# Kernel tuning notes

Measured on AMD Instinct MI355X. Metric: run time of the kernel, lower is better.

The kernel has to match this reference:

```python
import jax, jax.numpy as jnp
import numpy as np

# Model dims (match init_kwargs)
HID = 1024   # hidden_size
H   = 16     # num_heads
DK  = 64     # head_dim (key)
DV  = 128    # head value dim = int(head_dim * expand_v)
VAL = H * DV # value_dim = 2048
CONV = 4     # short conv kernel size
EPS = 1e-6
NORM_EPS = 1e-5


def _causal_conv_silu(x, w):
    # x: [B,T,C], w: [C,K] depthwise causal conv, no bias, silu activation
    T = x.shape[1]
    K = w.shape[1]
    xp = jnp.pad(x, ((0, 0), (K - 1, 0), (0, 0)))
    y = sum(xp[:, i:i + T, :] * w[:, i] for i in range(K))
    return jax.nn.silu(y)


def setup_inputs() -> dict:
    key = jax.random.key(0)
    ks = jax.random.split(key, 16)
    s = 0.02
    rn = lambda k, sh: jax.random.normal(k, sh, jnp.float32)
    return {
        'hidden_states': rn(ks[0], (1, 2048, HID)),
        'norm_w': jnp.ones((HID,), jnp.float32),
        'q_w': rn(ks[1], (H * DK, HID)) * s,
        'k_w': rn(ks[2], (H * DK, HID)) * s,
        'v_w': rn(ks[3], (VAL, HID)) * s,
        'a_w': rn(ks[4], (H, HID)) * s,
        'b_w': rn(ks[5], (H, HID)) * s,
        'g_w': rn(ks[6], (VAL, HID)) * s,
        'dt_bias': jax.random.uniform(ks[7], (H,), jnp.float32, -2.0, 0.0),
        'A_log': jnp.log(jax.random.uniform(ks[8], (H,), jnp.float32, 1.0, 8.0)),
        'conv_q_w': rn(ks[9], (H * DK, CONV)) * 0.2,
        'conv_k_w': rn(ks[10], (H * DK, CONV)) * 0.2,
        'conv_v_w': rn(ks[11], (VAL, CONV)) * 0.2,
        'o_norm_w': jnp.ones((DV,), jnp.float32),
        'o_proj_w': rn(ks[12], (HID, VAL)) * s,
        'out_proj_w': rn(ks[13], (HID, HID)) * s,
    }


def reference(hidden_states, norm_w, q_w, k_w, v_w, a_w, b_w, g_w, dt_bias,
              A_log, conv_q_w, conv_k_w, conv_v_w, o_norm_w, o_proj_w, out_proj_w):
    B, T, D = hidden_states.shape
    # RMSNorm
    x = hidden_states * jax.lax.rsqrt(
        jnp.mean(hidden_states * hidden_states, -1, keepdims=True) + EPS) * norm_w

    # projections + causal depthwise short conv + silu
    q = _causal_conv_silu(x @ q_w.T, conv_q_w).reshape(B, T, H, DK)
    k = _causal_conv_silu(x @ k_w.T, conv_k_w).reshape(B, T, H, DK)
    v = _causal_conv_silu(x @ v_w.T, conv_v_w).reshape(B, T, H, DV)

    beta = jax.nn.sigmoid(x @ b_w.T)                       # [B,T,H]
    g = -jnp.exp(A_log) * jax.nn.softplus(x @ a_w.T + dt_bias)  # [B,T,H] log-decay

    # rank-1 DC removal on keys: (I - 1 1^T / DK) k, i.e. subtract per-head mean
    k = k - jnp.mean(k, -1, keepdims=True)

    # L2 normalize q, k along head dim; scale q
    q = q * jax.lax.rsqrt(jnp.sum(q * q, -1, keepdims=True) + EPS)
    k = k * jax.lax.rsqrt(jnp.sum(k * k, -1, keepdims=True) + EPS)
    q = q * (DK ** -0.5)

    # gated delta-rule recurrence over time (time-major scan)
    qT = q.transpose(1, 0, 2, 3)
    kT = k.transpose(1, 0, 2, 3)
    vT = v.transpose(1, 0, 2, 3)
    bT = beta.transpose(1, 0, 2)
    gT = g.transpose(1, 0, 2)

    def step(S, inp):
        qt, kt, vt, bt, gt = inp              # S: [B,H,DK,DV]
        S = S * jnp.exp(gt)[..., None, None]
        v_new = (vt - jnp.einsum('bhk,bhkv->bhv', kt, S)) * bt[..., None]
        S = S + jnp.einsum('bhk,bhv->bhkv', kt, v_new)
        o = jnp.einsum('bhk,bhkv->bhv', qt, S)
        return S, o

    S0 = jnp.zeros((B, H, DK, DV), x.dtype)
    _, oT = jax.lax.scan(step, S0, (qT, kT, vT, bT, gT))
    o = oT.transpose(1, 0, 2, 3)                           # [B,T,H,DV]

    # gated RMSNorm on output heads
    gate = (x @ g_w.T).reshape(B, T, H, DV)
    o = o * jax.lax.rsqrt(jnp.mean(o * o, -1, keepdims=True) + NORM_EPS) * o_norm_w
    o = o * jax.nn.silu(gate)

    o = o.reshape(B, T, VAL) @ o_proj_w.T                  # [B,T,HID]
    return o @ out_proj_w.T
```

## Files before the change

kernel.cpp:

```cpp
#include <hip/hip_runtime.h>
#include <math.h>

#define TT 2048
#define S72 72

typedef __bf16 bf16;
typedef __bf16 bf16x8 __attribute__((ext_vector_type(8)));
typedef __bf16 bf16x4v __attribute__((ext_vector_type(4)));
typedef __bf16 bf16x2v __attribute__((ext_vector_type(2)));
typedef float f32x4 __attribute__((ext_vector_type(4)));

__device__ __forceinline__ float wredsum(float v) {
#pragma unroll
  for (int off = 32; off > 0; off >>= 1) v += __shfl_xor(v, off, 64);
  return v;
}
__device__ __forceinline__ float sigmoidf_(float x) { return 1.f / (1.f + __expf(-x)); }

__global__ __launch_bounds__(256) void k_rmsnorm(const float* __restrict__ h,
    const float* __restrict__ nw, const float* __restrict__ aw,
    const float* __restrict__ bw, const float* __restrict__ dtb,
    const float* __restrict__ alog, bf16* __restrict__ xb,
    float* __restrict__ graw, float* __restrict__ btb) {
  int t = blockIdx.x, tid = threadIdx.x;
  float4 hv = *(const float4*)(h + (size_t)t*1024 + tid*4);
  float ss = hv.x*hv.x + hv.y*hv.y + hv.z*hv.z + hv.w*hv.w;
  __shared__ float red[4];
  __shared__ __align__(16) float xs[1024];
  float wsum = wredsum(ss);
  if ((tid & 63) == 0) red[tid >> 6] = wsum;
  __syncthreads();
  float tot = red[0] + red[1] + red[2] + red[3];
  float rs = rsqrtf(tot * (1.f/1024.f) + 1e-6f);
  float4 w4 = *(const float4*)(nw + tid*4);
  float4 y;
  y.x = hv.x*rs*w4.x; y.y = hv.y*rs*w4.y; y.z = hv.z*rs*w4.z; y.w = hv.w*rs*w4.w;
  *(float4*)(xs + tid*4) = y;
  bf16x4v b; b[0]=(bf16)y.x; b[1]=(bf16)y.y; b[2]=(bf16)y.z; b[3]=(bf16)y.w;
  *(bf16x4v*)(xb + (size_t)t*1024 + tid*4) = b;
  __syncthreads();
  int wave = tid >> 6, lane = tid & 63;
  const float4* x4 = (const float4*)xs;
#pragma unroll
  for (int hi = 0; hi < 4; ++hi) {
    int hh = wave*4 + hi;
    float sa = 0.f, sb = 0.f;
#pragma unroll
    for (int i = 0; i < 4; ++i) {
      float4 xv = x4[i*64 + lane];
      float4 av = *(const float4*)(aw + hh*1024 + i*256 + lane*4);
      float4 bv = *(const float4*)(bw + hh*1024 + i*256 + lane*4);
      sa += xv.x*av.x + xv.y*av.y + xv.z*av.z + xv.w*av.w;
      sb += xv.x*bv.x + xv.y*bv.y + xv.z*bv.z + xv.w*bv.w;
    }
    sa = wredsum(sa); sb = wredsum(sb);
    if (lane == 0) {
      float ap = sa + dtb[hh];
      float sp = (ap > 20.f) ? ap : log1pf(expf(ap));
      graw[t*16 + hh] = -expf(alog[hh]) * sp;
      btb[t*16 + hh] = 1.f / (1.f + expf(-sb));
    }
  }
}

__global__ void k_castw(const float* __restrict__ qw, const float* __restrict__ kw,
    const float* __restrict__ vw, const float* __restrict__ gw,
    const float* __restrict__ opw, const float* __restrict__ ow,
    bf16* qwb, bf16* kwb, bf16* vwb, bf16* gwb, bf16* opwb, bf16* owb) {
  for (long u = (long)blockIdx.x*256 + threadIdx.x; u < 2359296; u += (long)gridDim.x*256) {
    const float* src; bf16* dst; long l;
    if      (u <  262144) { src=qw;  dst=qwb;  l=u; }
    else if (u <  524288) { src=kw;  dst=kwb;  l=u-262144; }
    else if (u < 1048576) { src=vw;  dst=vwb;  l=u-524288; }
    else if (u < 1572864) { src=gw;  dst=gwb;  l=u-1048576; }
    else if (u < 2097152) { src=opw; dst=opwb; l=u-1572864; }
    else                  { src=ow;  dst=owb;  l=u-2097152; }
    float4 s = *(const float4*)(src + l*4);
    bf16x4v b; b[0]=(bf16)s.x; b[1]=(bf16)s.y; b[2]=(bf16)s.z; b[3]=(bf16)s.w;
    *(bf16x4v*)(dst + l*4) = b;
  }
}

template <typename OutT>
__device__ __forceinline__ void gemm_body(const bf16* __restrict__ A,
    const bf16* __restrict__ B, OutT* __restrict__ C, int N, int K, int m0, int n0) {
  __shared__ bf16 As[2][128*32];
  __shared__ bf16 Bs[2][128*32];
  const int tid = threadIdx.x, lane = tid & 63, wave = tid >> 6;
  const int wm = (wave >> 1) * 64, wn = (wave & 1) * 64;
  const int srow = wave*16 + (lane >> 2);
  const int swl = (((lane & 3) ^ ((lane >> 3) & 3))) * 8;
  const int sdst = (lane & 3) * 8;
  const int quad = lane >> 4, l16 = lane & 15;
  const int sw = (l16 >> 1) & 3;
  f32x4 acc[4][4] = {};
  const int nk = K >> 5;
#pragma unroll
  for (int i = 0; i < 2; ++i) {
    int r = i*64 + srow;
    __builtin_amdgcn_global_load_lds(
      (__attribute__((address_space(1))) void*)(A + (size_t)(m0 + r)*K + swl),
      (__attribute__((address_space(3))) void*)(&As[0][r*32 + sdst]), 16, 0, 0);
    __builtin_amdgcn_global_load_lds(
      (__attribute__((address_space(1))) void*)(B + (size_t)(n0 + r)*K + swl),
      (__attribute__((address_space(3))) void*)(&Bs[0][r*32 + sdst]), 16, 0, 0);
  }
  for (int kt = 0; kt < nk; ++kt) {
    const int cur = kt & 1;
    __syncthreads();
    bf16x8 af[4], bfr[4];
#pragma unroll
    for (int mt = 0; mt < 4; ++mt)
      af[mt] = *(const bf16x8*)(&As[cur][(wm + mt*16 + l16)*32 + (quad ^ sw)*8]);
#pragma unroll
    for (int nt = 0; nt < 4; ++nt)
      bfr[nt] = *(const bf16x8*)(&Bs[cur][(wn + nt*16 + l16)*32 + (quad ^ sw)*8]);
    if (kt + 1 < nk) {
      int k0 = (kt + 1) << 5;
#pragma unroll
      for (int i = 0; i < 2; ++i) {
        int r = i*64 + srow;
        __builtin_amdgcn_global_load_lds(
          (__attribute__((address_space(1))) void*)(A + (size_t)(m0 + r)*K + k0 + swl),
          (__attribute__((address_space(3))) void*)(&As[cur^1][r*32 + sdst]), 16, 0, 0);
        __builtin_amdgcn_global_load_lds(
          (__attribute__((address_space(1))) void*)(B + (size_t)(n0 + r)*K + k0 + swl),
          (__attribute__((address_space(3))) void*)(&Bs[cur^1][r*32 + sdst]), 16, 0, 0);
      }
    }
#pragma unroll
    for (int mt = 0; mt < 4; ++mt)
#pragma unroll
      for (int nt = 0; nt < 4; ++nt)
        acc[mt][nt] = __builtin_amdgcn_mfma_f32_16x16x32_bf16(af[mt], bfr[nt], acc[mt][nt], 0, 0, 0);
  }
#pragma unroll
  for (int mt = 0; mt < 4; ++mt)
#pragma unroll
    for (int nt = 0; nt < 4; ++nt)
#pragma unroll
      for (int r = 0; r < 4; ++r) {
        int row = m0 + wm + mt*16 + quad*4 + r;
        int col = n0 + wn + nt*16 + l16;
        C[(size_t)row*N + col] = (OutT)acc[mt][nt][r];
      }
}

__global__ __launch_bounds__(256) void k_gemm_proj(const bf16* __restrict__ A,
    const bf16* __restrict__ qwb, const bf16* __restrict__ kwb,
    const bf16* __restrict__ vwb, const bf16* __restrict__ gwb,
    bf16* __restrict__ qpre, bf16* __restrict__ kpre,
    bf16* __restrict__ vpre, bf16* __restrict__ gpre) {
  int bx = blockIdx.x;
  const bf16* B; bf16* C; int N, xt;
  if      (bx <  8) { B = qwb; C = qpre; N = 1024; xt = bx; }
  else if (bx < 16) { B = kwb; C = kpre; N = 1024; xt = bx - 8; }
  else if (bx < 32) { B = vwb; C = vpre; N = 2048; xt = bx - 16; }
  else              { B = gwb; C = gpre; N = 2048; xt = bx - 32; }
  gemm_body<bf16>(A, B, C, N, 1024, blockIdx.y*128, xt*128);
}

template <typename OutT>
__global__ __launch_bounds__(256) void k_gemm_bt(const bf16* __restrict__ A,
    const bf16* __restrict__ B, OutT* __restrict__ C, int N, int K) {
  gemm_body<OutT>(A, B, C, N, K, blockIdx.y*128, blockIdx.x*128);
}

template<int NT>
__device__ __forceinline__ void mm_band(const bf16* A_lds, const bf16* B_lds,
    int w16, int cb, int l16, int quad, f32x4* acc) {
#pragma unroll
  for (int n = 0; n < NT; ++n) { acc[n][0]=0.f; acc[n][1]=0.f; acc[n][2]=0.f; acc[n][3]=0.f; }
#pragma unroll
  for (int kt = 0; kt < 2; ++kt) {
    bf16x8 af = *(const bf16x8*)(A_lds + (w16 + l16)*S72 + kt*32 + quad*8);
#pragma unroll
    for (int n = 0; n < NT; ++n) {
      bf16x8 bf = *(const bf16x8*)(B_lds + (cb + n*16 + l16)*S72 + kt*32 + quad*8);
      acc[n] = __builtin_amdgcn_mfma_f32_16x16x32_bf16(af, bf, acc[n], 0, 0, 0);
    }
  }
}

__global__ __launch_bounds__(512) void k_prepass(
    const bf16* __restrict__ qpre, const bf16* __restrict__ kpre,
    const bf16* __restrict__ vpre, const float* __restrict__ cqw,
    const float* __restrict__ ckw, const float* __restrict__ cvw,
    const float* __restrict__ graw, const float* __restrict__ beta,
    bf16* __restrict__ EF, float* __restrict__ dSl, float* __restrict__ obuf) {
  const int bx = blockIdx.x, c = bx >> 4, h = bx & 15, tid = threadIdx.x;
  const int t0 = c * 64;
  const int wave = tid >> 6, lane = tid & 63, l16 = lane & 15, quad = lane >> 4;
  const int w16 = (wave >> 1) * 16;
  const int chh = wave & 1;
  const int r0 = wave * 8;

  __shared__ bf16 SM[50688];
  __shared__ float qf[64*68];
  __shared__ float bs[64], bts_s[64], es[64], gms[64];
  bf16* Kr    = SM;
  bf16* KT    = SM + 4608;
  bf16* KbT   = SM + 9216;
  bf16* Pm    = SM + 13824;
  bf16* powR0 = SM + 18432;
  bf16* powT0 = SM + 23040;
  bf16* powR1 = SM + 27648;
  bf16* powT1 = SM + 32256;
  bf16* prod0 = SM + 36864;
  bf16* prod1 = SM + 41472;
  bf16* T2T   = SM + 46080;
  bf16* VT    = SM + 18432;
  bf16* VlT   = SM + 27648;

  if (tid < 64) {
    float g = graw[(size_t)(t0 + tid)*16 + h];
    float b = g;
#pragma unroll
    for (int off = 1; off < 64; off <<= 1) {
      float p = __shfl_up(b, off, 64);
      if (tid >= off) b += p;
    }
    bs[tid] = b;
    bts_s[tid] = beta[(size_t)(t0 + tid)*16 + h];
    float b63 = __shfl(b, 63, 64);
    es[tid] = __expf(b63 - b);
    gms[tid] = __expf(b);
  }

  float kreg[8], vreg[16];
  {
    float4 wq  = *(const float4*)(cqw + (h*64 + lane)*4);
    float4 wk  = *(const float4*)(ckw + (h*64 + lane)*4);
    float tv[11];
#pragma unroll
    for (int j = 0; j < 11; ++j) {
      int tg = t0 + r0 + j - 3;
      tv[j] = (tg >= 0) ? (float)qpre[(size_t)tg*1024 + h*64 + lane] : 0.f;
    }
#pragma unroll
    for (int rr = 0; rr < 8; ++rr) {
      float y = tv[rr]*wq.x + tv[rr+1]*wq.y + tv[rr+2]*wq.z + tv[rr+3]*wq.w;
      y = y * sigmoidf_(y);
      float ssq = wredsum(y*y);
      y *= rsqrtf(ssq + 1e-6f) * 0.125f;
      qf[(r0+rr)*68 + lane] = y;
    }
#pragma unroll
    for (int j = 0; j < 11; ++j) {
      int tg = t0 + r0 + j - 3;
      tv[j] = (tg >= 0) ? (float)kpre[(size_t)tg*1024 + h*64 + lane] : 0.f;
    }
#pragma unroll
    for (int rr = 0; rr < 8; ++rr) {
      float y = tv[rr]*wk.x + tv[rr+1]*wk.y + tv[rr+2]*wk.z + tv[rr+3]*wk.w;
      y = y * sigmoidf_(y);
      float m = wredsum(y) * (1.f/64.f);
      y -= m;
      float ssq = wredsum(y*y);
      y *= rsqrtf(ssq + 1e-6f);
      kreg[rr] = y;
      bf16 kb = (bf16)y;
      Kr[(r0+rr)*S72 + lane] = kb;
      KT[lane*S72 + (r0+rr)] = kb;
    }
#pragma unroll
    for (int hf = 0; hf < 2; ++hf) {
      float4 wv = *(const float4*)(cvw + (h*128 + hf*64 + lane)*4);
#pragma unroll
      for (int j = 0; j < 11; ++j) {
        int tg = t0 + r0 + j - 3;
        tv[j] = (tg >= 0) ? (float)vpre[(size_t)tg*2048 + h*128 + hf*64 + lane] : 0.f;
      }
#pragma unroll
      for (int rr = 0; rr < 8; ++rr) {
        float y = tv[rr]*wv.x + tv[rr+1]*wv.y + tv[rr+2]*wv.z + tv[rr+3]*wv.w;
        vreg[hf*8+rr] = y * sigmoidf_(y);
      }
    }
  }
  __syncthreads();
#pragma unroll
  for (int rr = 0; rr < 8; ++rr)
    KbT[lane*S72 + (r0+rr)] = (bf16)(kreg[rr] * es[r0+rr]);

  {
    f32x4 acc[2];
    mm_band<2>(Kr, Kr, w16, chh*32, l16, quad, acc);
#pragma unroll
    for (int n = 0; n < 2; ++n) {
      int col = chh*32 + n*16 + l16;
      bf16x4v tv;
#pragma unroll
      for (int r = 0; r < 4; ++r) {
        int row = w16 + quad*4 + r;
        float nv = 0.f;
        if (row > col) nv = -bts_s[row] * __expf(bs[row] - bs[col]) * acc[n][r];
        bf16 nb = (bf16)nv;
        powR0[row*S72 + col] = nb;
        tv[r] = nb;
        prod0[row*S72 + col] = (row == col) ? (bf16)1.f : nb;
      }
      *(bf16x4v*)(powT0 + col*S72 + w16 + quad*4) = tv;
    }
  }
  {
    f32x4 acc[2];
#pragma unroll
    for (int n = 0; n < 2; ++n) { acc[n][0]=0.f; acc[n][1]=0.f; acc[n][2]=0.f; acc[n][3]=0.f; }
#pragma unroll
    for (int kt = 0; kt < 2; ++kt) {
      const float* qp = qf + (w16 + l16)*68 + kt*32 + quad*8;
      float4 a4 = *(const float4*)qp;
      float4 b4 = *(const float4*)(qp + 4);
      bf16x8 af;
      af[0]=(bf16)a4.x; af[1]=(bf16)a4.y; af[2]=(bf16)a4.z; af[3]=(bf16)a4.w;
      af[4]=(bf16)b4.x; af[5]=(bf16)b4.y; af[6]=(bf16)b4.z; af[7]=(bf16)b4.w;
#pragma unroll
      for (int n = 0; n < 2; ++n) {
        bf16x8 bf = *(const bf16x8*)(Kr + (chh*32 + n*16 + l16)*S72 + kt*32 + quad*8);
        acc[n] = __builtin_amdgcn_mfma_f32_16x16x32_bf16(af, bf, acc[n], 0, 0, 0);
      }
    }
#pragma unroll
    for (int n = 0; n < 2; ++n) {
      int col = chh*32 + n*16 + l16;
#pragma unroll
      for (int r = 0; r < 4; ++r) {
        int row = w16 + quad*4 + r;
        float pv = (row >= col) ? __expf(bs[row] - bs[col]) * acc[n][r] : 0.f;
        Pm[row*S72 + col] = (bf16)pv;
      }
    }
  }
  __syncthreads();

  int pc = 0, rc = 0;
#pragma unroll 1
  for (int i = 1; i <= 5; ++i) {
    bf16* sqA = pc ? powR1 : powR0;
    bf16* sqB = pc ? powT1 : powT0;
    bf16* sqRo = pc ? powR0 : powR1;
    bf16* sqTo = pc ? powT0 : powT1;
    {
      f32x4 acc[2];
      mm_band<2>(sqA, sqB, w16, chh*32, l16, quad, acc);
#pragma unroll
      for (int n = 0; n < 2; ++n) {
        int col = chh*32 + n*16 + l16;
        bf16x4v tv;
#pragma unroll
        for (int r = 0; r < 4; ++r) {
          int row = w16 + quad*4 + r;
          bf16 vb = (bf16)acc[n][r];
          sqRo[row*S72 + col] = vb;
          tv[r] = vb;
        }
        *(bf16x4v*)(sqTo + col*S72 + w16 + quad*4) = tv;
      }
    }
    __syncthreads();
    bf16* prA = rc ? prod1 : prod0;
    bf16* prO = rc ? prod0 : prod1;
    {
      f32x4 acc[2];
      mm_band<2>(prA, sqTo, w16, chh*32, l16, quad, acc);
#pragma unroll
      for (int n = 0; n < 2; ++n) {
        int col = chh*32 + n*16 + l16;
        bf16x4v tv;
#pragma unroll
        for (int r = 0; r < 4; ++r) {
          int row = w16 + quad*4 + r;
          float val = acc[n][r] + (float)prA[row*S72 + col];
          prO[row*S72 + col] = (bf16)val;
          tv[r] = (bf16)(val * bts_s[col] * gms[col]);
        }
        if (i == 5) *(bf16x4v*)(T2T + col*S72 + w16 + quad*4) = tv;
      }
    }
    __syncthreads();
    pc ^= 1; rc ^= 1;
  }
  bf16* Mrow = rc ? prod1 : prod0;
  bf16* WR   = rc ? prod0 : prod1;

#pragma unroll
  for (int hf = 0; hf < 2; ++hf)
#pragma unroll
    for (int rr = 0; rr < 8; ++rr)
      VT[(hf*64 + lane)*S72 + (r0+rr)] = (bf16)(bts_s[r0+rr] * vreg[hf*8+rr]);
  __syncthreads();

  {
    f32x4 acc[4];
    mm_band<4>(Mrow, VT, w16, chh*64, l16, quad, acc);
#pragma unroll
    for (int n = 0; n < 4; ++n) {
      int col = chh*64 + n*16 + l16;
      bf16x4v tv;
#pragma unroll
      for (int r = 0; r < 4; ++r) tv[r] = (bf16)acc[n][r];
      *(bf16x4v*)(VlT + col*S72 + w16 + quad*4) = tv;
    }
  }
  __syncthreads();

  {
    f32x4 acc[4];
    mm_band<4>(KbT, VlT, w16, chh*64, l16, quad, acc);
#pragma unroll
    for (int n = 0; n < 4; ++n) {
      int col = chh*64 + n*16 + l16;
#pragma unroll
      for (int r = 0; r < 4; ++r)
        dSl[(size_t)bx*8192 + (size_t)(w16 + quad*4 + r)*128 + col] = acc[n][r];
    }
  }
  {
    f32x4 acc[2];
    mm_band<2>(KbT, T2T, w16, chh*32, l16, quad, acc);
#pragma unroll
    for (int n = 0; n < 2; ++n) {
      int col = chh*32 + n*16 + l16;
#pragma unroll
      for (int r = 0; r < 4; ++r)
        WR[(w16 + quad*4 + r)*S72 + col] = (bf16)acc[n][r];
    }
  }
  __syncthreads();
  {
    f32x4 acc[2];
    mm_band<2>(WR, KT, w16, chh*32, l16, quad, acc);
    float gC = gms[63];
    size_t eb = (size_t)bx * 13824;
#pragma unroll
    for (int n = 0; n < 2; ++n) {
      int col = chh*32 + n*16 + l16;
#pragma unroll
      for (int r = 0; r < 4; ++r) {
        int row = w16 + quad*4 + r;
        float ev = ((row == col) ? gC : 0.f) - acc[n][r];
        bf16 eh = (bf16)ev;
        EF[eb + row*S72 + col] = eh;
        EF[eb + 4608 + row*S72 + col] = (bf16)(ev - (float)eh);
      }
    }
  }
  __syncthreads();
  {
    f32x4 acc[2];
    mm_band<2>(Pm, T2T, w16, chh*32, l16, quad, acc);
#pragma unroll
    for (int n = 0; n < 2; ++n) {
      int col = chh*32 + n*16 + l16;
#pragma unroll
      for (int r = 0; r < 4; ++r)
        WR[(w16 + quad*4 + r)*S72 + col] = (bf16)acc[n][r];
    }
  }
  __syncthreads();
  {
    f32x4 acc[2];
    mm_band<2>(WR, KT, w16, chh*32, l16, quad, acc);
    size_t eb = (size_t)bx * 13824;
#pragma unroll
    for (int n = 0; n < 2; ++n) {
      int col = chh*32 + n*16 + l16;
#pragma unroll
      for (int r = 0; r < 4; ++r) {
        int row = w16 + quad*4 + r;
        float qv = qf[row*68 + col];
        EF[eb + 9216 + row*S72 + col] = (bf16)(gms[row]*qv - acc[n][r]);
      }
    }
  }
  {
    f32x4 acc[4];
    mm_band<4>(Pm, VlT, w16, chh*64, l16, quad, acc);
#pragma unroll
    for (int n = 0; n < 4; ++n) {
      int col = chh*64 + n*16 + l16;
#pragma unroll
      for (int r = 0; r < 4; ++r)
        obuf[(size_t)(t0 + w16 + quad*4 + r)*2048 + h*128 + col] = acc[n][r];
    }
  }
}

__global__ __launch_bounds__(256) void k_seq(const bf16* __restrict__ EF,
    const float* __restrict__ dSl, float* __restrict__ osb) {
  const int h = blockIdx.x >> 2, dq = blockIdx.x & 3;
  const int tid = threadIdx.x, wave = tid >> 6, lane = tid & 63;
  const int l16 = lane & 15, quad = lane >> 4;
  const int mb = wave * 16;
  __shared__ bf16 ebuf[2][13824];
  __shared__ bf16 Sthi[32*S72], Stlo[32*S72];
  for (int i = tid; i < 2304; i += 256) { Sthi[i] = (bf16)0.f; Stlo[i] = (bf16)0.f; }
  {
    const bf16* efg = EF + (size_t)h * 13824;
    for (int i = tid; i < 1728; i += 256)
      __builtin_amdgcn_global_load_lds(
        (__attribute__((address_space(1))) void*)(efg + i*8),
        (__attribute__((address_space(3))) void*)(&ebuf[0][i*8]), 16, 0, 0);
  }
  float dsv[8];
  {
    size_t base = (size_t)h*8192 + dq*32;
#pragma unroll
    for (int nt = 0; nt < 2; ++nt)
#pragma unroll
      for (int r = 0; r < 4; ++r)
        dsv[nt*4+r] = dSl[base + (size_t)(mb + quad*4 + r)*128 + nt*16 + l16];
  }
  __syncthreads();
#pragma unroll 1
  for (int c = 0; c < 32; ++c) {
    const int cur = c & 1, nxt = cur ^ 1;
    float dsn[8] = {};
    if (c + 1 < 32) {
      const bf16* efg = EF + (size_t)((c+1)*16 + h) * 13824;
      for (int i = tid; i < 1728; i += 256)
        __builtin_amdgcn_global_load_lds(
          (__attribute__((address_space(1))) void*)(efg + i*8),
          (__attribute__((address_space(3))) void*)(&ebuf[nxt][i*8]), 16, 0, 0);
      size_t base = (size_t)((c+1)*16 + h)*8192 + dq*32;
#pragma unroll
      for (int nt = 0; nt < 2; ++nt)
#pragma unroll
        for (int r = 0; r < 4; ++r)
          dsn[nt*4+r] = dSl[base + (size_t)(mb + quad*4 + r)*128 + nt*16 + l16];
    }
    const bf16* Eh = &ebuf[cur][0];
    const bf16* El = &ebuf[cur][4608];
    const bf16* Ff = &ebuf[cur][9216];
    bf16x8 bh[2][2], bl[2][2];
#pragma unroll
    for (int nt = 0; nt < 2; ++nt)
#pragma unroll
      for (int kt = 0; kt < 2; ++kt) {
        bh[nt][kt] = *(const bf16x8*)(Sthi + (nt*16 + l16)*S72 + kt*32 + quad*8);
        bl[nt][kt] = *(const bf16x8*)(Stlo + (nt*16 + l16)*S72 + kt*32 + quad*8);
      }
    f32x4 accS[2], accO[2];
#pragma unroll
    for (int nt = 0; nt < 2; ++nt) {
#pragma unroll
      for (int r = 0; r < 4; ++r) accS[nt][r] = dsv[nt*4+r];
      accO[nt][0]=0.f; accO[nt][1]=0.f; accO[nt][2]=0.f; accO[nt][3]=0.f;
    }
#pragma unroll
    for (int kt = 0; kt < 2; ++kt) {
      bf16x8 aeh = *(const bf16x8*)(Eh + (mb + l16)*S72 + kt*32 + quad*8);
      bf16x8 ael = *(const bf16x8*)(El + (mb + l16)*S72 + kt*32 + quad*8);
      bf16x8 aff = *(const bf16x8*)(Ff + (mb + l16)*S72 + kt*32 + quad*8);
#pragma unroll
      for (int nt = 0; nt < 2; ++nt) {
        accS[nt] = __builtin_amdgcn_mfma_f32_16x16x32_bf16(aeh, bh[nt][kt], accS[nt], 0, 0, 0);
        accS[nt] = __builtin_amdgcn_mfma_f32_16x16x32_bf16(aeh, bl[nt][kt], accS[nt], 0, 0, 0);
        accS[nt] = __builtin_amdgcn_mfma_f32_16x16x32_bf16(ael, bh[nt][kt], accS[nt], 0, 0, 0);
        accO[nt] = __builtin_amdgcn_mfma_f32_16x16x32_bf16(aff, bh[nt][kt], accO[nt], 0, 0, 0);
        accO[nt] = __builtin_amdgcn_mfma_f32_16x16x32_bf16(aff, bl[nt][kt], accO[nt], 0, 0, 0);
      }
    }
    __syncthreads();
    {
      int t0 = c*64;
#pragma unroll
      for (int nt = 0; nt < 2; ++nt)
#pragma unroll
        for (int r = 0; r < 4; ++r)
          osb[(size_t)(t0 + mb + quad*4 + r)*2048 + h*128 + dq*32 + nt*16 + l16] = accO[nt][r];
    }
#pragma unroll
    for (int nt = 0; nt < 2; ++nt) {
      bf16x4v hv, lv;
#pragma unroll
      for (int r = 0; r < 4; ++r) {
        float v = accS[nt][r];
        bf16 hb = (bf16)v;
        hv[r] = hb;
        lv[r] = (bf16)(v - (float)hb);
      }
      *(bf16x4v*)(Sthi + (nt*16 + l16)*S72 + mb + quad*4) = hv;
      *(bf16x4v*)(Stlo + (nt*16 + l16)*S72 + mb + quad*4) = lv;
    }
#pragma unroll
    for (int i = 0; i < 8; ++i) dsv[i] = dsn[i];
    __syncthreads();
  }
}

__global__ __launch_bounds__(64) void k_gatenorm(const float* __restrict__ o,
    const float* __restrict__ os, const bf16* __restrict__ gpre,
    const float* __restrict__ onw, bf16* __restrict__ og) {
  int t = blockIdx.x, hh = blockIdx.y, lane = threadIdx.x;
  size_t base = (size_t)t*2048 + hh*128 + lane*2;
  float2 o2 = *(const float2*)(o + base);
  float2 s2 = *(const float2*)(os + base);
  o2.x += s2.x; o2.y += s2.y;
  float ss = wredsum(o2.x*o2.x + o2.y*o2.y);
  float rs = rsqrtf(ss * (1.f/128.f) + 1e-5f);
  float2 nw = *(const float2*)(onw + lane*2);
  bf16x2v g2 = *(const bf16x2v*)(gpre + base);
  float g0 = (float)g2[0], g1 = (float)g2[1];
  float r0 = o2.x * rs * nw.x * (g0 * sigmoidf_(g0));
  float r1 = o2.y * rs * nw.y * (g1 * sigmoidf_(g1));
  bf16x2v b; b[0] = (bf16)r0; b[1] = (bf16)r1;
  *(bf16x2v*)(og + base) = b;
}

extern "C" void kernel_launch(void* const* d_in, const int* in_sizes, int n_in,
                              void* d_out, int out_size, void* d_ws, size_t ws_size,
                              hipStream_t stream) {
  const float* hs   = (const float*)d_in[0];
  const float* nw   = (const float*)d_in[1];
  const float* qw   = (const float*)d_in[2];
  const float* kw   = (const float*)d_in[3];
  const float* vw   = (const float*)d_in[4];
  const float* aw   = (const float*)d_in[5];
  const float* bw   = (const float*)d_in[6];
  const float* gw   = (const float*)d_in[7];
  const float* dtb  = (const float*)d_in[8];
  const float* alog = (const float*)d_in[9];
  const float* cqw  = (const float*)d_in[10];
  const float* ckw  = (const float*)d_in[11];
  const float* cvw  = (const float*)d_in[12];
  const float* onw  = (const float*)d_in[13];
  const float* opw  = (const float*)d_in[14];
  const float* ow   = (const float*)d_in[15];
  float* out = (float*)d_out;

  char* p = (char*)d_ws;
  auto alloc = [&](size_t bytes) { char* r = p; p += (bytes + 255) & ~255ull; return r; };
  bf16*  xb    = (bf16*) alloc((size_t)2048*1024*2);
  bf16*  qwb   = (bf16*) alloc((size_t)1024*1024*2);
  bf16*  kwb   = (bf16*) alloc((size_t)1024*1024*2);
  bf16*  vwb   = (bf16*) alloc((size_t)2048*1024*2);
  bf16*  gwb   = (bf16*) alloc((size_t)2048*1024*2);
  bf16*  opwb  = (bf16*) alloc((size_t)1024*2048*2);
  bf16*  owb   = (bf16*) alloc((size_t)1024*1024*2);
  bf16*  qpre  = (bf16*) alloc((size_t)2048*1024*2);
  bf16*  kpre  = (bf16*) alloc((size_t)2048*1024*2);
  bf16*  vpre  = (bf16*) alloc((size_t)2048*2048*2);
  bf16*  gpre  = (bf16*) alloc((size_t)2048*2048*2);
  float* graw  = (float*)alloc((size_t)2048*16*4);
  float* btb   = (float*)alloc((size_t)2048*16*4);
  float* ob    = (float*)alloc((size_t)2048*2048*4);
  bf16*  ogb   = (bf16*) alloc((size_t)2048*2048*2);
  bf16*  h1b   = (bf16*) alloc((size_t)2048*1024*2);
  bf16*  EF    = (bf16*) alloc((size_t)512*13824*2);
  float* osb   = (float*)alloc((size_t)512*8192*4);
  float* dSl   = (float*)xb;

  k_rmsnorm<<<2048, 256, 0, stream>>>(hs, nw, aw, bw, dtb, alog, xb, graw, btb);
  k_castw<<<4608, 256, 0, stream>>>(qw, kw, vw, gw, opw, ow, qwb, kwb, vwb, gwb, opwb, owb);
  k_gemm_proj<<<dim3(48,16,1), 256, 0, stream>>>(xb, qwb, kwb, vwb, gwb, qpre, kpre, vpre, gpre);
  k_prepass<<<512, 512, 0, stream>>>(qpre, kpre, vpre, cqw, ckw, cvw, graw, btb, EF, dSl, ob);
  k_seq<<<64, 256, 0, stream>>>(EF, dSl, osb);
  k_gatenorm<<<dim3(2048,16,1), 64, 0, stream>>>(ob, osb, gpre, onw, ogb);
  k_gemm_bt<bf16><<<dim3(8,16,1), 256, 0, stream>>>(ogb, opwb, h1b, 1024, 2048);
  k_gemm_bt<float><<<dim3(8,16,1), 256, 0, stream>>>(h1b, owb, out, 1024, 1024);
}
```

Measured before the change: 311.9 us.

## Merge rmsnorm and weight cast, swizzle prepass LDS, use 128x64 output GEMM tiles

Merges the rmsnorm and weight-cast kernels into a single launch to save one kernel launch. The prepass kernel now uses XOR-swizzled 64-wide LDS layouts instead of 72-stride padding, stores q as bf16 instead of float, and reorders its stages so buffers can be reused, which reduces shared memory per block and may raise occupancy. The two output-projection GEMMs move to a new 128x64 tile kernel, doubling the grid to 256 blocks for better CU coverage. The costs are extra rounding of q to bf16 before the QK product and smaller per-block reuse in the output GEMMs.

```diff
diff --git a/kernel.cpp b/kernel.cpp
--- a/kernel.cpp
+++ b/kernel.cpp
@@ -1,7 +1,6 @@
 #include <hip/hip_runtime.h>
 #include <math.h>
 
-#define TT 2048
 #define S72 72
 
 typedef __bf16 bf16;
@@ -17,16 +16,44 @@
 }
 __device__ __forceinline__ float sigmoidf_(float x) { return 1.f / (1.f + __expf(-x)); }
 
-__global__ __launch_bounds__(256) void k_rmsnorm(const float* __restrict__ h,
+__device__ __forceinline__ int sxy(int row, int col) {
+  return (row << 6) + ((((col >> 3) ^ (row & 7)) << 3) | (col & 7));
+}
+__device__ __forceinline__ int sx8(int row, int chunk) {
+  return (row << 6) + ((chunk ^ (row & 7)) << 3);
+}
+
+__global__ __launch_bounds__(256) void k_pre(const float* __restrict__ h,
     const float* __restrict__ nw, const float* __restrict__ aw,
     const float* __restrict__ bw, const float* __restrict__ dtb,
     const float* __restrict__ alog, bf16* __restrict__ xb,
-    float* __restrict__ graw, float* __restrict__ btb) {
-  int t = blockIdx.x, tid = threadIdx.x;
+    float* __restrict__ graw, float* __restrict__ btb,
+    const float* __restrict__ qw, const float* __restrict__ kw,
+    const float* __restrict__ vw, const float* __restrict__ gw,
+    const float* __restrict__ opw, const float* __restrict__ ow,
+    bf16* qwb, bf16* kwb, bf16* vwb, bf16* gwb, bf16* opwb, bf16* owb) {
+  __shared__ float red[4];
+  __shared__ __align__(16) float xs[1024];
+  int tid = threadIdx.x;
+  if (blockIdx.x >= 2048) {
+    long cb = blockIdx.x - 2048;
+    for (long u = cb*256 + tid; u < 2359296; u += 4608l*256) {
+      const float* src; bf16* dst; long l;
+      if      (u <  262144) { src=qw;  dst=qwb;  l=u; }
+      else if (u <  524288) { src=kw;  dst=kwb;  l=u-262144; }
+      else if (u < 1048576) { src=vw;  dst=vwb;  l=u-524288; }
+      else if (u < 1572864) { src=gw;  dst=gwb;  l=u-1048576; }
+      else if (u < 2097152) { src=opw; dst=opwb; l=u-1572864; }
+      else                  { src=ow;  dst=owb;  l=u-2097152; }
+      float4 s = *(const float4*)(src + l*4);
+      bf16x4v b; b[0]=(bf16)s.x; b[1]=(bf16)s.y; b[2]=(bf16)s.z; b[3]=(bf16)s.w;
+      *(bf16x4v*)(dst + l*4) = b;
+    }
+    return;
+  }
+  int t = blockIdx.x;
   float4 hv = *(const float4*)(h + (size_t)t*1024 + tid*4);
   float ss = hv.x*hv.x + hv.y*hv.y + hv.z*hv.z + hv.w*hv.w;
-  __shared__ float red[4];
-  __shared__ __align__(16) float xs[1024];
   float wsum = wredsum(ss);
   if ((tid & 63) == 0) red[tid >> 6] = wsum;
   __syncthreads();
@@ -60,24 +87,6 @@
       graw[t*16 + hh] = -expf(alog[hh]) * sp;
       btb[t*16 + hh] = 1.f / (1.f + expf(-sb));
     }
-  }
-}
-
-__global__ void k_castw(const float* __restrict__ qw, const float* __restrict__ kw,
-    const float* __restrict__ vw, const float* __restrict__ gw,
-    const float* __restrict__ opw, const float* __restrict__ ow,
-    bf16* qwb, bf16* kwb, bf16* vwb, bf16* gwb, bf16* opwb, bf16* owb) {
-  for (long u = (long)blockIdx.x*256 + threadIdx.x; u < 2359296; u += (long)gridDim.x*256) {
-    const float* src; bf16* dst; long l;
-    if      (u <  262144) { src=qw;  dst=qwb;  l=u; }
-    else if (u <  524288) { src=kw;  dst=kwb;  l=u-262144; }
-    else if (u < 1048576) { src=vw;  dst=vwb;  l=u-524288; }
-    else if (u < 1572864) { src=gw;  dst=gwb;  l=u-1048576; }
-    else if (u < 2097152) { src=opw; dst=opwb; l=u-1572864; }
-    else                  { src=ow;  dst=owb;  l=u-2097152; }
-    float4 s = *(const float4*)(src + l*4);
-    bf16x4v b; b[0]=(bf16)s.x; b[1]=(bf16)s.y; b[2]=(bf16)s.z; b[3]=(bf16)s.w;
-    *(bf16x4v*)(dst + l*4) = b;
   }
 }
 
@@ -161,9 +170,69 @@
 }
 
 template <typename OutT>
-__global__ __launch_bounds__(256) void k_gemm_bt(const bf16* __restrict__ A,
+__global__ __launch_bounds__(256) void k_gemm_bt64(const bf16* __restrict__ A,
     const bf16* __restrict__ B, OutT* __restrict__ C, int N, int K) {
-  gemm_body<OutT>(A, B, C, N, K, blockIdx.y*128, blockIdx.x*128);
+  __shared__ bf16 As[2][128*32];
+  __shared__ bf16 Bs[2][64*32];
+  const int tid = threadIdx.x, lane = tid & 63, wave = tid >> 6;
+  const int wm = wave * 32;
+  const int srow = wave*16 + (lane >> 2);
+  const int swl = (((lane & 3) ^ ((lane >> 3) & 3))) * 8;
+  const int sdst = (lane & 3) * 8;
+  const int quad = lane >> 4, l16 = lane & 15;
+  const int sw = (l16 >> 1) & 3;
+  const int m0 = blockIdx.y * 128, n0 = blockIdx.x * 64;
+  f32x4 acc[2][4] = {};
+  const int nk = K >> 5;
+#pragma unroll
+  for (int i = 0; i < 2; ++i) {
+    int r = i*64 + srow;
+    __builtin_amdgcn_global_load_lds(
+      (__attribute__((address_space(1))) void*)(A + (size_t)(m0 + r)*K + swl),
+      (__attribute__((address_space(3))) void*)(&As[0][r*32 + sdst]), 16, 0, 0);
+  }
+  __builtin_amdgcn_global_load_lds(
+    (__attribute__((address_space(1))) void*)(B + (size_t)(n0 + srow)*K + swl),
+    (__attribute__((address_space(3))) void*)(&Bs[0][srow*32 + sdst]), 16, 0, 0);
+  for (int kt = 0; kt < nk; ++kt) {
+    const int cur = kt & 1;
+    __syncthreads();
+    bf16x8 af[2], bfr[4];
+#pragma unroll
+    for (int mt = 0; mt < 2; ++mt)
+      af[mt] = *(const bf16x8*)(&As[cur][(wm + mt*16 + l16)*32 + (quad ^ sw)*8]);
+#pragma unroll
+    for (int nt = 0; nt < 4; ++nt)
+      bfr[nt] = *(const bf16x8*)(&Bs[cur][(nt*16 + l16)*32 + (quad ^ sw)*8]);
+    if (kt + 1 < nk) {
+      int k0 = (kt + 1) << 5;
+#pragma unroll
+      for (int i = 0; i < 2; ++i) {
+        int r = i*64 + srow;
+        __builtin_amdgcn_global_load_lds(
+          (__attribute__((address_space(1))) void*)(A + (size_t)(m0 + r)*K + k0 + swl),
+          (__attribute__((address_space(3))) void*)(&As[cur^1][r*32 + sdst]), 16, 0, 0);
+      }
+      __builtin_amdgcn_global_load_lds(
+        (__attribute__((address_space(1))) void*)(B + (size_t)(n0 + srow)*K + k0 + swl),
+        (__attribute__((address_space(3))) void*)(&Bs[cur^1][srow*32 + sdst]), 16, 0, 0);
+    }
+#pragma unroll
+    for (int mt = 0; mt < 2; ++mt)
+#pragma unroll
+      for (int nt = 0; nt < 4; ++nt)
+        acc[mt][nt] = __builtin_amdgcn_mfma_f32_16x16x32_bf16(af[mt], bfr[nt], acc[mt][nt], 0, 0, 0);
+  }
+#pragma unroll
+  for (int mt = 0; mt < 2; ++mt)
+#pragma unroll
+    for (int nt = 0; nt < 4; ++nt)
+#pragma unroll
+      for (int r = 0; r < 4; ++r) {
+        int row = m0 + wm + mt*16 + quad*4 + r;
+        int col = n0 + nt*16 + l16;
+        C[(size_t)row*N + col] = (OutT)acc[mt][nt][r];
+      }
 }
 
 template<int NT>
@@ -173,10 +242,10 @@
   for (int n = 0; n < NT; ++n) { acc[n][0]=0.f; acc[n][1]=0.f; acc[n][2]=0.f; acc[n][3]=0.f; }
 #pragma unroll
   for (int kt = 0; kt < 2; ++kt) {
-    bf16x8 af = *(const bf16x8*)(A_lds + (w16 + l16)*S72 + kt*32 + quad*8);
+    bf16x8 af = *(const bf16x8*)(A_lds + sx8(w16 + l16, kt*4 + quad));
 #pragma unroll
     for (int n = 0; n < NT; ++n) {
-      bf16x8 bf = *(const bf16x8*)(B_lds + (cb + n*16 + l16)*S72 + kt*32 + quad*8);
+      bf16x8 bf = *(const bf16x8*)(B_lds + sx8(cb + n*16 + l16, kt*4 + quad));
       acc[n] = __builtin_amdgcn_mfma_f32_16x16x32_bf16(af, bf, acc[n], 0, 0, 0);
     }
   }
@@ -195,22 +264,24 @@
   const int chh = wave & 1;
   const int r0 = wave * 8;
 
-  __shared__ bf16 SM[50688];
-  __shared__ float qf[64*68];
+  __shared__ bf16 SM[36864];
   __shared__ float bs[64], bts_s[64], es[64], gms[64];
   bf16* Kr    = SM;
-  bf16* KT    = SM + 4608;
-  bf16* KbT   = SM + 9216;
-  bf16* Pm    = SM + 13824;
-  bf16* powR0 = SM + 18432;
-  bf16* powT0 = SM + 23040;
-  bf16* powR1 = SM + 27648;
-  bf16* powT1 = SM + 32256;
-  bf16* prod0 = SM + 36864;
-  bf16* prod1 = SM + 41472;
-  bf16* T2T   = SM + 46080;
-  bf16* VT    = SM + 18432;
-  bf16* VlT   = SM + 27648;
+  bf16* powR0 = SM + 4096;
+  bf16* prod0 = SM + 8192;
+  bf16* T2T   = SM + 12288;
+  bf16* powT0 = SM + 16384;
+  bf16* powR1 = SM + 20480;
+  bf16* powT1 = SM + 24576;
+  bf16* prod1 = SM + 28672;
+  bf16* qbf   = SM + 32768;
+  bf16* VT   = SM;
+  bf16* VlT  = SM + 8192;
+  bf16* KT   = powT0;
+  bf16* KbT  = powR1;
+  bf16* Pm   = powT1;
+  bf16* WR   = prod0;
+  bf16* Mrow = prod1;
 
   if (tid < 64) {
     float g = graw[(size_t)(t0 + tid)*16 + h];
@@ -243,7 +314,7 @@
       y = y * sigmoidf_(y);
       float ssq = wredsum(y*y);
       y *= rsqrtf(ssq + 1e-6f) * 0.125f;
-      qf[(r0+rr)*68 + lane] = y;
+      qbf[sxy(r0+rr, lane)] = (bf16)y;
     }
 #pragma unroll
     for (int j = 0; j < 11; ++j) {
@@ -259,9 +330,7 @@
       float ssq = wredsum(y*y);
       y *= rsqrtf(ssq + 1e-6f);
       kreg[rr] = y;
-      bf16 kb = (bf16)y;
-      Kr[(r0+rr)*S72 + lane] = kb;
-      KT[lane*S72 + (r0+rr)] = kb;
+      Kr[sxy(r0+rr, lane)] = (bf16)y;
     }
 #pragma unroll
     for (int hf = 0; hf < 2; ++hf) {
@@ -279,9 +348,6 @@
     }
   }
   __syncthreads();
-#pragma unroll
-  for (int rr = 0; rr < 8; ++rr)
-    KbT[lane*S72 + (r0+rr)] = (bf16)(kreg[rr] * es[r0+rr]);
 
   {
     f32x4 acc[2];
@@ -296,40 +362,11 @@
         float nv = 0.f;
         if (row > col) nv = -bts_s[row] * __expf(bs[row] - bs[col]) * acc[n][r];
         bf16 nb = (bf16)nv;
-        powR0[row*S72 + col] = nb;
+        powR0[sxy(row, col)] = nb;
         tv[r] = nb;
-        prod0[row*S72 + col] = (row == col) ? (bf16)1.f : nb;
-      }
-      *(bf16x4v*)(powT0 + col*S72 + w16 + quad*4) = tv;
-    }
-  }
-  {
-    f32x4 acc[2];
-#pragma unroll
-    for (int n = 0; n < 2; ++n) { acc[n][0]=0.f; acc[n][1]=0.f; acc[n][2]=0.f; acc[n][3]=0.f; }
-#pragma unroll
-    for (int kt = 0; kt < 2; ++kt) {
-      const float* qp = qf + (w16 + l16)*68 + kt*32 + quad*8;
-      float4 a4 = *(const float4*)qp;
-      float4 b4 = *(const float4*)(qp + 4);
-      bf16x8 af;
-      af[0]=(bf16)a4.x; af[1]=(bf16)a4.y; af[2]=(bf16)a4.z; af[3]=(bf16)a4.w;
-      af[4]=(bf16)b4.x; af[5]=(bf16)b4.y; af[6]=(bf16)b4.z; af[7]=(bf16)b4.w;
-#pragma unroll
-      for (int n = 0; n < 2; ++n) {
-        bf16x8 bf = *(const bf16x8*)(Kr + (chh*32 + n*16 + l16)*S72 + kt*32 + quad*8);
-        acc[n] = __builtin_amdgcn_mfma_f32_16x16x32_bf16(af, bf, acc[n], 0, 0, 0);
-      }
-    }
-#pragma unroll
-    for (int n = 0; n < 2; ++n) {
-      int col = chh*32 + n*16 + l16;
-#pragma unroll
-      for (int r = 0; r < 4; ++r) {
-        int row = w16 + quad*4 + r;
-        float pv = (row >= col) ? __expf(bs[row] - bs[col]) * acc[n][r] : 0.f;
-        Pm[row*S72 + col] = (bf16)pv;
-      }
+        prod0[sxy(row, col)] = (row == col) ? (bf16)1.f : nb;
+      }
+      *(bf16x4v*)(powT0 + sxy(col, w16 + quad*4)) = tv;
     }
   }
   __syncthreads();
@@ -352,10 +389,10 @@
         for (int r = 0; r < 4; ++r) {
           int row = w16 + quad*4 + r;
           bf16 vb = (bf16)acc[n][r];
-          sqRo[row*S72 + col] = vb;
+          sqRo[sxy(row, col)] = vb;
           tv[r] = vb;
         }
-        *(bf16x4v*)(sqTo + col*S72 + w16 + quad*4) = tv;
+        *(bf16x4v*)(sqTo + sxy(col, w16 + quad*4)) = tv;
       }
     }
     __syncthreads();
@@ -371,51 +408,48 @@
 #pragma unroll
         for (int r = 0; r < 4; ++r) {
           int row = w16 + quad*4 + r;
-          float val = acc[n][r] + (float)prA[row*S72 + col];
-          prO[row*S72 + col] = (bf16)val;
+          float val = acc[n][r] + (float)prA[sxy(row, col)];
+          prO[sxy(row, col)] = (bf16)val;
           tv[r] = (bf16)(val * bts_s[col] * gms[col]);
         }
-        if (i == 5) *(bf16x4v*)(T2T + col*S72 + w16 + quad*4) = tv;
+        if (i == 5) *(bf16x4v*)(T2T + sxy(col, w16 + quad*4)) = tv;
       }
     }
     __syncthreads();
     pc ^= 1; rc ^= 1;
   }
-  bf16* Mrow = rc ? prod1 : prod0;
-  bf16* WR   = rc ? prod0 : prod1;
-
-#pragma unroll
-  for (int hf = 0; hf < 2; ++hf)
-#pragma unroll
-    for (int rr = 0; rr < 8; ++rr)
-      VT[(hf*64 + lane)*S72 + (r0+rr)] = (bf16)(bts_s[r0+rr] * vreg[hf*8+rr]);
-  __syncthreads();
-
-  {
-    f32x4 acc[4];
-    mm_band<4>(Mrow, VT, w16, chh*64, l16, quad, acc);
-#pragma unroll
-    for (int n = 0; n < 4; ++n) {
-      int col = chh*64 + n*16 + l16;
-      bf16x4v tv;
-#pragma unroll
-      for (int r = 0; r < 4; ++r) tv[r] = (bf16)acc[n][r];
-      *(bf16x4v*)(VlT + col*S72 + w16 + quad*4) = tv;
-    }
-  }
-  __syncthreads();
-
-  {
-    f32x4 acc[4];
-    mm_band<4>(KbT, VlT, w16, chh*64, l16, quad, acc);
-#pragma unroll
-    for (int n = 0; n < 4; ++n) {
-      int col = chh*64 + n*16 + l16;
-#pragma unroll
-      for (int r = 0; r < 4; ++r)
-        dSl[(size_t)bx*8192 + (size_t)(w16 + quad*4 + r)*128 + col] = acc[n][r];
-    }
-  }
+
+#pragma unroll
+  for (int rr = 0; rr < 8; ++rr) {
+    KT[sxy(lane, r0+rr)]  = (bf16)kreg[rr];
+    KbT[sxy(lane, r0+rr)] = (bf16)(kreg[rr] * es[r0+rr]);
+  }
+  {
+    f32x4 acc[2];
+#pragma unroll
+    for (int n = 0; n < 2; ++n) { acc[n][0]=0.f; acc[n][1]=0.f; acc[n][2]=0.f; acc[n][3]=0.f; }
+#pragma unroll
+    for (int kt = 0; kt < 2; ++kt) {
+      bf16x8 af = *(const bf16x8*)(qbf + sx8(w16 + l16, kt*4 + quad));
+#pragma unroll
+      for (int n = 0; n < 2; ++n) {
+        bf16x8 bf = *(const bf16x8*)(Kr + sx8(chh*32 + n*16 + l16, kt*4 + quad));
+        acc[n] = __builtin_amdgcn_mfma_f32_16x16x32_bf16(af, bf, acc[n], 0, 0, 0);
+      }
+    }
+#pragma unroll
+    for (int n = 0; n < 2; ++n) {
+      int col = chh*32 + n*16 + l16;
+#pragma unroll
+      for (int r = 0; r < 4; ++r) {
+        int row = w16 + quad*4 + r;
+        float pv = (row >= col) ? __expf(bs[row] - bs[col]) * acc[n][r] : 0.f;
+        Pm[sxy(row, col)] = (bf16)pv;
+      }
+    }
+  }
+  __syncthreads();
+
   {
     f32x4 acc[2];
     mm_band<2>(KbT, T2T, w16, chh*32, l16, quad, acc);
@@ -424,9 +458,14 @@
       int col = chh*32 + n*16 + l16;
 #pragma unroll
       for (int r = 0; r < 4; ++r)
-        WR[(w16 + quad*4 + r)*S72 + col] = (bf16)acc[n][r];
-    }
-  }
+        WR[sxy(w16 + quad*4 + r, col)] = (bf16)acc[n][r];
+    }
+  }
+#pragma unroll
+  for (int hf = 0; hf < 2; ++hf)
+#pragma unroll
+    for (int rr = 0; rr < 8; ++rr)
+      VT[sxy(hf*64 + lane, r0+rr)] = (bf16)(bts_s[r0+rr] * vreg[hf*8+rr]);
   __syncthreads();
   {
     f32x4 acc[2];
@@ -455,7 +494,7 @@
       int col = chh*32 + n*16 + l16;
 #pragma unroll
       for (int r = 0; r < 4; ++r)
-        WR[(w16 + quad*4 + r)*S72 + col] = (bf16)acc[n][r];
+        WR[sxy(w16 + quad*4 + r, col)] = (bf16)acc[n][r];
     }
   }
   __syncthreads();
@@ -469,9 +508,34 @@
 #pragma unroll
       for (int r = 0; r < 4; ++r) {
         int row = w16 + quad*4 + r;
-        float qv = qf[row*68 + col];
+        float qv = (float)qbf[sxy(row, col)];
         EF[eb + 9216 + row*S72 + col] = (bf16)(gms[row]*qv - acc[n][r]);
       }
+    }
+  }
+  __syncthreads();
+  {
+    f32x4 acc[4];
+    mm_band<4>(Mrow, VT, w16, chh*64, l16, quad, acc);
+#pragma unroll
+    for (int n = 0; n < 4; ++n) {
+      int col = chh*64 + n*16 + l16;
+      bf16x4v tv;
+#pragma unroll
+      for (int r = 0; r < 4; ++r) tv[r] = (bf16)acc[n][r];
+      *(bf16x4v*)(VlT + sxy(col, w16 + quad*4)) = tv;
+    }
+  }
+  __syncthreads();
+  {
+    f32x4 acc[4];
+    mm_band<4>(KbT, VlT, w16, chh*64, l16, quad, acc);
+#pragma unroll
+    for (int n = 0; n < 4; ++n) {
+      int col = chh*64 + n*16 + l16;
+#pragma unroll
+      for (int r = 0; r < 4; ++r)
+        dSl[(size_t)bx*8192 + (size_t)(w16 + quad*4 + r)*128 + col] = acc[n][r];
     }
   }
   {
@@ -652,12 +716,13 @@
   float* osb   = (float*)alloc((size_t)512*8192*4);
   float* dSl   = (float*)xb;
 
-  k_rmsnorm<<<2048, 256, 0, stream>>>(hs, nw, aw, bw, dtb, alog, xb, graw, btb);
-  k_castw<<<4608, 256, 0, stream>>>(qw, kw, vw, gw, opw, ow, qwb, kwb, vwb, gwb, opwb, owb);
+  k_pre<<<2048+4608, 256, 0, stream>>>(hs, nw, aw, bw, dtb, alog, xb, graw, btb,
+                                       qw, kw, vw, gw, opw, ow,
+                                       qwb, kwb, vwb, gwb, opwb, owb);
   k_gemm_proj<<<dim3(48,16,1), 256, 0, stream>>>(xb, qwb, kwb, vwb, gwb, qpre, kpre, vpre, gpre);
   k_prepass<<<512, 512, 0, stream>>>(qpre, kpre, vpre, cqw, ckw, cvw, graw, btb, EF, dSl, ob);
   k_seq<<<64, 256, 0, stream>>>(EF, dSl, osb);
   k_gatenorm<<<dim3(2048,16,1), 64, 0, stream>>>(ob, osb, gpre, onw, ogb);
-  k_gemm_bt<bf16><<<dim3(8,16,1), 256, 0, stream>>>(ogb, opwb, h1b, 1024, 2048);
-  k_gemm_bt<float><<<dim3(8,16,1), 256, 0, stream>>>(h1b, owb, out, 1024, 1024);
-}
+  k_gemm_bt64<bf16><<<dim3(16,16,1), 256, 0, stream>>>(ogb, opwb, h1b, 1024, 2048);
+  k_gemm_bt64<float><<<dim3(16,16,1), 256, 0, stream>>>(h1b, owb, out, 1024, 1024);
+}
```

Result: faster. 286.2 us (-8.2%).
